# Kernel tuning notes

Measured on AMD Instinct MI355X. Metric: run time of the kernel, lower is better.

The kernel has to match this reference:

```python
import jax, jax.numpy as jnp
import numpy as np

T, B, FEAT, H, NC, ED = 64, 256, 924, 512, 151, 100
DROP_P = 0.2

def setup_inputs() -> dict:
    key = jax.random.key(0)
    ks = jax.random.split(key, 9)
    s_in = 1.0 / np.sqrt(FEAT + ED)
    s_st = 1.0 / np.sqrt(H)
    x = jax.random.normal(ks[0], (T, B, FEAT), dtype=jnp.float32)
    labels = jax.random.randint(ks[1], (T, B), 0, NC, dtype=jnp.int32)
    embed = jax.random.normal(ks[2], (NC, ED), dtype=jnp.float32)
    Wi = jax.random.normal(ks[3], (6 * H, FEAT + ED), dtype=jnp.float32) * s_in
    bi = jnp.zeros((6 * H,), dtype=jnp.float32)
    Ws = jax.random.normal(ks[4], (5 * H, H), dtype=jnp.float32) * s_st
    # state bias: forget-gate block initialized to 1.0 (as in reset_parameters)
    bs = jnp.zeros((5 * H,), dtype=jnp.float32).at[H:2 * H].set(1.0)
    Wo = jax.random.normal(ks[5], (NC, H), dtype=jnp.float32) * s_st
    bo = jnp.zeros((NC,), dtype=jnp.float32)
    # recurrent dropout mask, sampled once and reused at every timestep
    mask = jax.random.bernoulli(ks[6], 1.0 - DROP_P, (B, H)).astype(jnp.float32) / (1.0 - DROP_P)
    return {"x": x, "labels": labels, "embed": embed, "Wi": Wi, "bi": bi,
            "Ws": Ws, "bs": bs, "Wo": Wo, "bo": bo, "mask": mask}

def _cell(x_t, lab_t, h, c, embed, Wi, bi, Ws, bs, mask):
    emb = embed[lab_t]                                     # (B, ED) teacher-forced previous embedding
    ti = jnp.concatenate([x_t, emb], axis=1)               # (B, FEAT+ED)
    pi = ti @ Wi.T + bi                                    # (B, 6H)
    ps = h @ Ws.T + bs                                     # (B, 5H)
    ig = jax.nn.sigmoid(pi[:, 0*H:1*H] + ps[:, 0*H:1*H])
    fg = jax.nn.sigmoid(pi[:, 1*H:2*H] + ps[:, 1*H:2*H])
    mi = jnp.tanh(pi[:, 2*H:3*H] + ps[:, 2*H:3*H])
    og = jax.nn.sigmoid(pi[:, 3*H:4*H] + ps[:, 3*H:4*H])
    c_new = ig * mi + fg * c
    out = og * jnp.tanh(c_new)
    hg = jax.nn.sigmoid(pi[:, 4*H:5*H] + ps[:, 4*H:5*H])   # highway gate
    out = hg * out + (1.0 - hg) * pi[:, 5*H:6*H]           # highway blend
    out = out * mask                                       # recurrent dropout
    return out, c_new

def reference(x, labels, embed, Wi, bi, Ws, bs, Wo, bo, mask):
    h0 = jnp.zeros((B, H), dtype=x.dtype)
    c0 = jnp.zeros((B, H), dtype=x.dtype)

    def step(carry, xs):
        h, c = carry
        x_t, lab_t = xs
        h_new, c_new = _cell(x_t, lab_t, h, c, embed, Wi, bi, Ws, bs, mask)
        pred = h_new @ Wo.T + bo                           # (B, NC)
        return (h_new, c_new), pred

    (_, _), out_dists = jax.lax.scan(step, (h0, c0), (x, labels))
    return out_dists                                       # (T, B, NC)
```

## Files before the change

### kernel.cpp

```cpp
#include <hip/hip_runtime.h>
#include <cstdint>
#include <cstddef>

#define TT 64
#define BB 256
#define FEAT 924
#define HH 512
#define NC 151
#define ED 100
#define KIN 1024
#define SIXH 3072
#define FIVEH 2560
#define MROWS (TT * BB)
#define RLDS 81920

typedef __bf16 bf16_t;
typedef __bf16 bf16x8 __attribute__((ext_vector_type(8)));
typedef float f32x4 __attribute__((ext_vector_type(4)));

typedef __attribute__((address_space(1))) const unsigned int* gptr_t;
typedef __attribute__((address_space(3))) unsigned int* lptr_t;

__device__ __forceinline__ void gload16(const void* g, void* l) {
  __builtin_amdgcn_global_load_lds((gptr_t)g, (lptr_t)l, 16, 0, 0);
}

__device__ __forceinline__ f32x4 mfma16(bf16x8 a, bf16x8 b, f32x4 c) {
  return __builtin_amdgcn_mfma_f32_16x16x32_bf16(a, b, c, 0, 0, 0);
}

__device__ __forceinline__ float fsig(float x) {
  return 1.f / (1.f + __expf(-x));
}
__device__ __forceinline__ float ftanh_(float x) {
  return 1.f - 2.f / (1.f + __expf(2.f * x));
}

__global__ void k_f2b(const float* __restrict__ in, bf16_t* __restrict__ out, int n) {
  int i = blockIdx.x * 256 + threadIdx.x;
  int stride = gridDim.x * 256;
  for (; i < n; i += stride) out[i] = (bf16_t)in[i];
}

__global__ void k_wopad(const float* __restrict__ wo, bf16_t* __restrict__ out) {
  int i = blockIdx.x * 256 + threadIdx.x;
  int r = i >> 9, k = i & 511;
  out[i] = (r < NC) ? (bf16_t)wo[r * HH + k] : (bf16_t)0.f;
}

__global__ void k_gather(const float* __restrict__ x, const int* __restrict__ lab,
                         const float* __restrict__ emb, bf16_t* __restrict__ ti) {
  int row = blockIdx.x;
  int t = threadIdx.x;
  int lb = lab[row];
  const float* xr = x + (size_t)row * FEAT;
  bf16_t* tr = ti + (size_t)row * KIN;
#pragma unroll
  for (int e = 0; e < 4; ++e) {
    int col = t + e * 256;
    float v = (col < FEAT) ? xr[col] : emb[lb * ED + (col - FEAT)];
    tr[col] = (bf16_t)v;
  }
}

template <typename CT>
__global__ __launch_bounds__(256)
void k_gemm(const bf16_t* __restrict__ A, const bf16_t* __restrict__ Bm,
            const float* __restrict__ bias, CT* __restrict__ C,
            int M, int N, int K, int ldc, int nstore) {
  __shared__ __align__(16) bf16_t As[128 * 64];
  __shared__ __align__(16) bf16_t Bs[128 * 64];
  const int tid = threadIdx.x;
  const int l = tid & 63;
  const int w = tid >> 6;
  const int wr = w >> 1, wc = w & 1;
  const int m0 = blockIdx.y * 128, n0 = blockIdx.x * 128;
  const int l15 = l & 15, lq = l >> 4;

  f32x4 acc[4][4] = {};

  for (int k0 = 0; k0 < K; k0 += 64) {
#pragma unroll
    for (int q = 0; q < 4; ++q) {
      int rig = q * 32 + w * 8 + (l >> 3);
      int kc = (l & 7) ^ (rig & 7);
      gload16(A + (size_t)(m0 + rig) * K + k0 + kc * 8, As + q * 2048 + w * 512);
      gload16(Bm + (size_t)(n0 + rig) * K + k0 + kc * 8, Bs + q * 2048 + w * 512);
    }
    __syncthreads();
#pragma unroll
    for (int ks = 0; ks < 2; ++ks) {
      bf16x8 af[4], bf[4];
#pragma unroll
      for (int m = 0; m < 4; ++m) {
        int row = wr * 64 + m * 16 + l15;
        int kcs = (ks * 4 + lq) ^ (row & 7);
        af[m] = *(const bf16x8*)(As + row * 64 + kcs * 8);
      }
#pragma unroll
      for (int n = 0; n < 4; ++n) {
        int row = wc * 64 + n * 16 + l15;
        int kcs = (ks * 4 + lq) ^ (row & 7);
        bf[n] = *(const bf16x8*)(Bs + row * 64 + kcs * 8);
      }
#pragma unroll
      for (int m = 0; m < 4; ++m)
#pragma unroll
        for (int n = 0; n < 4; ++n)
          acc[m][n] = mfma16(af[m], bf[n], acc[m][n]);
    }
    __syncthreads();
  }

#pragma unroll
  for (int n = 0; n < 4; ++n) {
    int ccol = n0 + wc * 64 + n * 16 + l15;
    if (ccol >= nstore) continue;
    float bv = bias[ccol];
#pragma unroll
    for (int m = 0; m < 4; ++m) {
      int crow = m0 + wr * 64 + m * 16 + lq * 4;
#pragma unroll
      for (int j = 0; j < 4; ++j)
        C[(size_t)(crow + j) * ldc + ccol] = (CT)(acc[m][n][j] + bv);
    }
  }
}

template <typename PIT>
__global__ __launch_bounds__(128)
void k_recur(const bf16_t* __restrict__ Wsb, const float* __restrict__ bs,
             const PIT* __restrict__ pi, const float* __restrict__ mask,
             bf16_t* __restrict__ Hs, unsigned* __restrict__ ctr) {
  extern __shared__ __align__(16) char smem[];
  bf16_t* Wl = (bf16_t*)smem;
  const int tid = threadIdx.x;
  const int l = tid & 63;
  const int w = tid >> 6;
  const int l15 = l & 15, lq = l >> 4;
  const int bq = blockIdx.x, jq = blockIdx.y;
  const int b0 = bq * 32, j0 = jq * 16;
  const int j = j0 + l15;
  const int brow = b0 + w * 16;
  unsigned* myctr = ctr + bq * 64;

  union U8 { unsigned long long q[2]; bf16x8 v; };
  union CV { bf16_t b; unsigned short u; };

  for (int s = w * 40; s < w * 40 + 40; ++s) {
    int g = s >> 4, kk = s & 15;
    bf16x8 frag = *(const bf16x8*)(Wsb + (size_t)(g * HH + j0 + l15) * HH + kk * 32 + lq * 8);
    *(bf16x8*)(Wl + (size_t)s * 512 + l * 8) = frag;
  }
  __syncthreads();

  float bsr[5];
#pragma unroll
  for (int g = 0; g < 5; ++g) bsr[g] = bs[g * HH + j];
  float mreg[4], creg[4] = {0.f, 0.f, 0.f, 0.f};
#pragma unroll
  for (int r = 0; r < 4; ++r)
    mreg[r] = mask[(size_t)(brow + lq * 4 + r) * HH + j];

  for (int t = 0; t < TT; ++t) {
    if (t > 0) {
      if (tid == 0) {
        unsigned tgt = 32u * (unsigned)t;
        while (__hip_atomic_load(myctr, __ATOMIC_RELAXED, __HIP_MEMORY_SCOPE_AGENT) < tgt)
          __builtin_amdgcn_s_sleep(1);
      }
      __syncthreads();
    }

    const bf16_t* hsrc = Hs + (size_t)t * BB * HH + (size_t)(brow + l15) * HH;
    U8 au[16];
#pragma unroll
    for (int kk = 0; kk < 16; ++kk) {
      unsigned long long* p = (unsigned long long*)(hsrc + kk * 32 + lq * 8);
      au[kk].q[0] = __hip_atomic_load(p, __ATOMIC_RELAXED, __HIP_MEMORY_SCOPE_AGENT);
      au[kk].q[1] = __hip_atomic_load(p + 1, __ATOMIC_RELAXED, __HIP_MEMORY_SCOPE_AGENT);
    }

    const PIT* pit = pi + (size_t)t * BB * SIXH;
    float pv[4][6];
#pragma unroll
    for (int r = 0; r < 4; ++r) {
      const PIT* prow = pit + (size_t)(brow + lq * 4 + r) * SIXH + j;
#pragma unroll
      for (int g = 0; g < 6; ++g) pv[r][g] = (float)prow[g * HH];
    }

    f32x4 acc[5] = {};
#pragma unroll
    for (int kk = 0; kk < 16; ++kk) {
      bf16x8 a = au[kk].v;
#pragma unroll
      for (int g = 0; g < 5; ++g) {
        bf16x8 bb = *(const bf16x8*)(Wl + (size_t)(g * 16 + kk) * 512 + l * 8);
        acc[g] = mfma16(a, bb, acc[g]);
      }
    }

    bf16_t* hnext = Hs + (size_t)(t + 1) * BB * HH;
#pragma unroll
    for (int r = 0; r < 4; ++r) {
      int b = brow + lq * 4 + r;
      float ig = fsig(pv[r][0] + acc[0][r] + bsr[0]);
      float fg = fsig(pv[r][1] + acc[1][r] + bsr[1]);
      float mi = ftanh_(pv[r][2] + acc[2][r] + bsr[2]);
      float og = fsig(pv[r][3] + acc[3][r] + bsr[3]);
      float hg = fsig(pv[r][4] + acc[4][r] + bsr[4]);
      float cn = ig * mi + fg * creg[r];
      creg[r] = cn;
      float o = og * ftanh_(cn);
      o = hg * o + (1.f - hg) * pv[r][5];
      o *= mreg[r];
      CV cv; cv.b = (bf16_t)o;
      __hip_atomic_store((unsigned short*)(hnext + (size_t)b * HH + j), cv.u,
                         __ATOMIC_RELAXED, __HIP_MEMORY_SCOPE_AGENT);
    }

    __syncthreads();
    if (tid == 0)
      __hip_atomic_fetch_add(myctr, 1u, __ATOMIC_RELAXED, __HIP_MEMORY_SCOPE_AGENT);
  }
}

extern "C" void kernel_launch(void* const* d_in, const int* in_sizes, int n_in,
                              void* d_out, int out_size, void* d_ws, size_t ws_size,
                              hipStream_t stream) {
  const float* x    = (const float*)d_in[0];
  const int*   lab  = (const int*)d_in[1];
  const float* emb  = (const float*)d_in[2];
  const float* Wi   = (const float*)d_in[3];
  const float* bi   = (const float*)d_in[4];
  const float* Ws   = (const float*)d_in[5];
  const float* bs   = (const float*)d_in[6];
  const float* Wo   = (const float*)d_in[7];
  const float* bo   = (const float*)d_in[8];
  const float* mask = (const float*)d_in[9];
  float* out = (float*)d_out;

  char* w = (char*)d_ws;
  size_t off = 0;
  auto take = [&](size_t bytes) {
    void* p = w + off;
    off += (bytes + 255) & ~(size_t)255;
    return p;
  };

  bf16_t*   TI   = (bf16_t*)take((size_t)MROWS * KIN * 2);
  bf16_t*   Wib  = (bf16_t*)take((size_t)SIXH * KIN * 2);
  bf16_t*   Wsb  = (bf16_t*)take((size_t)FIVEH * HH * 2);
  bf16_t*   Wob  = (bf16_t*)take((size_t)256 * HH * 2);
  bf16_t*   Hs   = (bf16_t*)take((size_t)(TT + 1) * BB * HH * 2);
  unsigned* ctrs = (unsigned*)take(8 * 64 * sizeof(unsigned));
  void* piPtr = w + off;
  size_t avail = (ws_size > off) ? (ws_size - off) : 0;

  bool pifp32 = avail >= (size_t)MROWS * SIXH * 4;
  bool pibf16 = !pifp32 && avail >= (size_t)MROWS * SIXH * 2;
  if (!pifp32 && !pibf16) {
    hipMemsetAsync(d_out, 0, (size_t)out_size * 4, stream);
    return;
  }

  k_f2b<<<dim3(1024), dim3(256), 0, stream>>>(Wi, Wib, SIXH * KIN);
  k_f2b<<<dim3(512), dim3(256), 0, stream>>>(Ws, Wsb, FIVEH * HH);
  k_wopad<<<dim3(512), dim3(256), 0, stream>>>(Wo, Wob);
  k_gather<<<dim3(MROWS), dim3(256), 0, stream>>>(x, lab, emb, TI);
  hipMemsetAsync(Hs, 0, (size_t)BB * HH * 2, stream);
  hipMemsetAsync(ctrs, 0, 8 * 64 * sizeof(unsigned), stream);

  dim3 rg(8, 32), rb(128);
  if (pifp32) {
    float* pi = (float*)piPtr;
    k_gemm<float><<<dim3(SIXH / 128, MROWS / 128), dim3(256), 0, stream>>>(
        TI, Wib, bi, pi, MROWS, SIXH, KIN, SIXH, SIXH);
    const float* piC = pi;
    hipFuncSetAttribute((const void*)k_recur<float>,
                        hipFuncAttributeMaxDynamicSharedMemorySize, RLDS);
    void* args[6] = {&Wsb, &bs, &piC, &mask, &Hs, &ctrs};
    hipError_t e = hipLaunchCooperativeKernel((void*)k_recur<float>, rg, rb, args,
                                              RLDS, stream);
    if (e != hipSuccess)
      k_recur<float><<<rg, rb, RLDS, stream>>>(Wsb, bs, piC, mask, Hs, ctrs);
  } else {
    bf16_t* pi = (bf16_t*)piPtr;
    k_gemm<bf16_t><<<dim3(SIXH / 128, MROWS / 128), dim3(256), 0, stream>>>(
        TI, Wib, bi, pi, MROWS, SIXH, KIN, SIXH, SIXH);
    const bf16_t* piC = pi;
    hipFuncSetAttribute((const void*)k_recur<bf16_t>,
                        hipFuncAttributeMaxDynamicSharedMemorySize, RLDS);
    void* args[6] = {&Wsb, &bs, &piC, &mask, &Hs, &ctrs};
    hipError_t e = hipLaunchCooperativeKernel((void*)k_recur<bf16_t>, rg, rb, args,
                                              RLDS, stream);
    if (e != hipSuccess)
      k_recur<bf16_t><<<rg, rb, RLDS, stream>>>(Wsb, bs, piC, mask, Hs, ctrs);
  }

  k_gemm<float><<<dim3(2, MROWS / 128), dim3(256), 0, stream>>>(
      Hs + (size_t)BB * HH, Wob, bo, out, MROWS, 256, HH, NC, NC);
}
```

Before: 654.2 us.

## Replace counter barrier with per-wave flags and double-buffered tiled h exchange

Replaces the per-batch-group atomic counter, which was polled by one thread and followed by __syncthreads, with per-wave flag slots that every wave polls with a wave-wide all-check. Each wave then publishes its flag right after its own h stores drain. The recurrent state is also written to a double-buffered, tile-blocked layout so the next step's A-fragment loads are contiguous. The step t=0 matmul and the Hs memset are skipped because h0 is zero, and the pi loads for the next step are prefetched into registers during the current step. This removes block-level barrier latency from the serial timestep chain, at the cost of extra register pressure and a second store per h element.

```diff
diff --git a/kernel.cpp b/kernel.cpp
--- a/kernel.cpp
+++ b/kernel.cpp
@@ -131,7 +131,8 @@
 __global__ __launch_bounds__(128)
 void k_recur(const bf16_t* __restrict__ Wsb, const float* __restrict__ bs,
              const PIT* __restrict__ pi, const float* __restrict__ mask,
-             bf16_t* __restrict__ Hs, unsigned* __restrict__ ctr) {
+             bf16_t* __restrict__ Hs, bf16_t* __restrict__ Hf2,
+             unsigned* __restrict__ ctr) {
   extern __shared__ __align__(16) char smem[];
   bf16_t* Wl = (bf16_t*)smem;
   const int tid = threadIdx.x;
@@ -142,10 +143,23 @@
   const int b0 = bq * 32, j0 = jq * 16;
   const int j = j0 + l15;
   const int brow = b0 + w * 16;
-  unsigned* myctr = ctr + bq * 64;
+  unsigned* flags = ctr + bq * 64;
 
   union U8 { unsigned long long q[2]; bf16x8 v; };
   union CV { bf16_t b; unsigned short u; };
+
+  float pvA[4][6], pvB[4][6];
+  auto loadpi = [&](int t, float (*pv)[6]) {
+    const PIT* pit = pi + (size_t)t * BB * SIXH;
+#pragma unroll
+    for (int r = 0; r < 4; ++r) {
+      const PIT* prow = pit + (size_t)(brow + lq * 4 + r) * SIXH + j;
+#pragma unroll
+      for (int g = 0; g < 6; ++g) pv[r][g] = (float)prow[g * HH];
+    }
+  };
+
+  loadpi(0, pvA);
 
   for (int s = w * 40; s < w * 40 + 40; ++s) {
     int g = s >> 4, kk = s & 15;
@@ -162,67 +176,76 @@
   for (int r = 0; r < 4; ++r)
     mreg[r] = mask[(size_t)(brow + lq * 4 + r) * HH + j];
 
+  const int myflag = jq * 2 + w;
+
   for (int t = 0; t < TT; ++t) {
+    f32x4 acc[5] = {};
+    U8 au[16];
+
     if (t > 0) {
-      if (tid == 0) {
-        unsigned tgt = 32u * (unsigned)t;
-        while (__hip_atomic_load(myctr, __ATOMIC_RELAXED, __HIP_MEMORY_SCOPE_AGENT) < tgt)
-          __builtin_amdgcn_s_sleep(1);
-      }
-      __syncthreads();
-    }
-
-    const bf16_t* hsrc = Hs + (size_t)t * BB * HH + (size_t)(brow + l15) * HH;
-    U8 au[16];
-#pragma unroll
-    for (int kk = 0; kk < 16; ++kk) {
-      unsigned long long* p = (unsigned long long*)(hsrc + kk * 32 + lq * 8);
-      au[kk].q[0] = __hip_atomic_load(p, __ATOMIC_RELAXED, __HIP_MEMORY_SCOPE_AGENT);
-      au[kk].q[1] = __hip_atomic_load(p + 1, __ATOMIC_RELAXED, __HIP_MEMORY_SCOPE_AGENT);
-    }
-
-    const PIT* pit = pi + (size_t)t * BB * SIXH;
-    float pv[4][6];
+      unsigned tgt = (unsigned)t;
+      while (true) {
+        unsigned v = __hip_atomic_load(flags + l, __ATOMIC_RELAXED, __HIP_MEMORY_SCOPE_AGENT);
+        if (__all((int)(v >= tgt))) break;
+        __builtin_amdgcn_s_sleep(1);
+      }
+
+      const bf16_t* hb = Hf2 + (size_t)(t & 1) * BB * HH + (size_t)bq * 16384
+                       + (size_t)(w * 16 + l15) * 32 + lq * 8;
+#pragma unroll
+      for (int kk = 0; kk < 16; ++kk) {
+        unsigned long long* p = (unsigned long long*)(hb + kk * 1024);
+        au[kk].q[0] = __hip_atomic_load(p, __ATOMIC_RELAXED, __HIP_MEMORY_SCOPE_AGENT);
+        au[kk].q[1] = __hip_atomic_load(p + 1, __ATOMIC_RELAXED, __HIP_MEMORY_SCOPE_AGENT);
+      }
+    }
+
+    if (t + 1 < TT) loadpi(t + 1, pvB);
+
+    if (t > 0) {
+#pragma unroll
+      for (int kk = 0; kk < 16; ++kk) {
+        bf16x8 a = au[kk].v;
+#pragma unroll
+        for (int g = 0; g < 5; ++g) {
+          bf16x8 bb = *(const bf16x8*)(Wl + (size_t)(g * 16 + kk) * 512 + l * 8);
+          acc[g] = mfma16(a, bb, acc[g]);
+        }
+      }
+    }
+
+    bf16_t* hsN = Hs + (size_t)(t + 1) * BB * HH;
+    bf16_t* hfN = Hf2 + (size_t)((t + 1) & 1) * BB * HH + (size_t)bq * 16384
+                + (size_t)(jq >> 1) * 1024 + (jq & 1) * 16 + l15;
 #pragma unroll
     for (int r = 0; r < 4; ++r) {
-      const PIT* prow = pit + (size_t)(brow + lq * 4 + r) * SIXH + j;
-#pragma unroll
-      for (int g = 0; g < 6; ++g) pv[r][g] = (float)prow[g * HH];
-    }
-
-    f32x4 acc[5] = {};
-#pragma unroll
-    for (int kk = 0; kk < 16; ++kk) {
-      bf16x8 a = au[kk].v;
-#pragma unroll
-      for (int g = 0; g < 5; ++g) {
-        bf16x8 bb = *(const bf16x8*)(Wl + (size_t)(g * 16 + kk) * 512 + l * 8);
-        acc[g] = mfma16(a, bb, acc[g]);
-      }
-    }
-
-    bf16_t* hnext = Hs + (size_t)(t + 1) * BB * HH;
-#pragma unroll
-    for (int r = 0; r < 4; ++r) {
-      int b = brow + lq * 4 + r;
-      float ig = fsig(pv[r][0] + acc[0][r] + bsr[0]);
-      float fg = fsig(pv[r][1] + acc[1][r] + bsr[1]);
-      float mi = ftanh_(pv[r][2] + acc[2][r] + bsr[2]);
-      float og = fsig(pv[r][3] + acc[3][r] + bsr[3]);
-      float hg = fsig(pv[r][4] + acc[4][r] + bsr[4]);
+      int row = w * 16 + lq * 4 + r;
+      int b = b0 + row;
+      float ig = fsig(pvA[r][0] + acc[0][r] + bsr[0]);
+      float fg = fsig(pvA[r][1] + acc[1][r] + bsr[1]);
+      float mi = ftanh_(pvA[r][2] + acc[2][r] + bsr[2]);
+      float og = fsig(pvA[r][3] + acc[3][r] + bsr[3]);
+      float hg = fsig(pvA[r][4] + acc[4][r] + bsr[4]);
       float cn = ig * mi + fg * creg[r];
       creg[r] = cn;
       float o = og * ftanh_(cn);
-      o = hg * o + (1.f - hg) * pv[r][5];
+      o = hg * o + (1.f - hg) * pvA[r][5];
       o *= mreg[r];
       CV cv; cv.b = (bf16_t)o;
-      __hip_atomic_store((unsigned short*)(hnext + (size_t)b * HH + j), cv.u,
+      hsN[(size_t)b * HH + j] = cv.b;
+      __hip_atomic_store((unsigned short*)(hfN + (size_t)row * 32), cv.u,
                          __ATOMIC_RELAXED, __HIP_MEMORY_SCOPE_AGENT);
     }
 
-    __syncthreads();
-    if (tid == 0)
-      __hip_atomic_fetch_add(myctr, 1u, __ATOMIC_RELAXED, __HIP_MEMORY_SCOPE_AGENT);
+    asm volatile("s_waitcnt vmcnt(0)" ::: "memory");
+    if (l == 0)
+      __hip_atomic_store(flags + myflag, (unsigned)(t + 1),
+                         __ATOMIC_RELAXED, __HIP_MEMORY_SCOPE_AGENT);
+
+#pragma unroll
+    for (int r = 0; r < 4; ++r)
+#pragma unroll
+      for (int g = 0; g < 6; ++g) pvA[r][g] = pvB[r][g];
   }
 }
 
@@ -254,6 +277,7 @@
   bf16_t*   Wsb  = (bf16_t*)take((size_t)FIVEH * HH * 2);
   bf16_t*   Wob  = (bf16_t*)take((size_t)256 * HH * 2);
   bf16_t*   Hs   = (bf16_t*)take((size_t)(TT + 1) * BB * HH * 2);
+  bf16_t*   Hf2  = (bf16_t*)take((size_t)2 * BB * HH * 2);
   unsigned* ctrs = (unsigned*)take(8 * 64 * sizeof(unsigned));
   void* piPtr = w + off;
   size_t avail = (ws_size > off) ? (ws_size - off) : 0;
@@ -269,7 +293,6 @@
   k_f2b<<<dim3(512), dim3(256), 0, stream>>>(Ws, Wsb, FIVEH * HH);
   k_wopad<<<dim3(512), dim3(256), 0, stream>>>(Wo, Wob);
   k_gather<<<dim3(MROWS), dim3(256), 0, stream>>>(x, lab, emb, TI);
-  hipMemsetAsync(Hs, 0, (size_t)BB * HH * 2, stream);
   hipMemsetAsync(ctrs, 0, 8 * 64 * sizeof(unsigned), stream);
 
   dim3 rg(8, 32), rb(128);
@@ -280,11 +303,11 @@
     const float* piC = pi;
     hipFuncSetAttribute((const void*)k_recur<float>,
                         hipFuncAttributeMaxDynamicSharedMemorySize, RLDS);
-    void* args[6] = {&Wsb, &bs, &piC, &mask, &Hs, &ctrs};
+    void* args[7] = {&Wsb, &bs, &piC, &mask, &Hs, &Hf2, &ctrs};
     hipError_t e = hipLaunchCooperativeKernel((void*)k_recur<float>, rg, rb, args,
                                               RLDS, stream);
     if (e != hipSuccess)
-      k_recur<float><<<rg, rb, RLDS, stream>>>(Wsb, bs, piC, mask, Hs, ctrs);
+      k_recur<float><<<rg, rb, RLDS, stream>>>(Wsb, bs, piC, mask, Hs, Hf2, ctrs);
   } else {
     bf16_t* pi = (bf16_t*)piPtr;
     k_gemm<bf16_t><<<dim3(SIXH / 128, MROWS / 128), dim3(256), 0, stream>>>(
@@ -292,11 +315,11 @@
     const bf16_t* piC = pi;
     hipFuncSetAttribute((const void*)k_recur<bf16_t>,
                         hipFuncAttributeMaxDynamicSharedMemorySize, RLDS);
-    void* args[6] = {&Wsb, &bs, &piC, &mask, &Hs, &ctrs};
+    void* args[7] = {&Wsb, &bs, &piC, &mask, &Hs, &Hf2, &ctrs};
     hipError_t e = hipLaunchCooperativeKernel((void*)k_recur<bf16_t>, rg, rb, args,
                                               RLDS, stream);
     if (e != hipSuccess)
-      k_recur<bf16_t><<<rg, rb, RLDS, stream>>>(Wsb, bs, piC, mask, Hs, ctrs);
+      k_recur<bf16_t><<<rg, rb, RLDS, stream>>>(Wsb, bs, piC, mask, Hs, Hf2, ctrs);
   }
 
   k_gemm<float><<<dim3(2, MROWS / 128), dim3(256), 0, stream>>>(
```

After: 783.0 us. 1.2x slower.
